# Performance work log

Hardware: AMD Instinct MI355X
Metric: run time of the kernel (lower is better)

The kernel has to match this reference:

```python
import jax, jax.numpy as jnp
import numpy as np

N, K, C_IN, C_OUT = 30000, 16, 128, 256


def setup_inputs() -> dict:
    key = jax.random.key(0)
    ks = jax.random.split(key, 8)
    s1 = 1.0 / np.sqrt(2 * C_IN)
    s2 = 1.0 / np.sqrt(C_OUT)
    s3 = 1.0 / np.sqrt(C_IN)
    return {
        "feat": jax.random.normal(ks[0], (N, C_IN), dtype=jnp.float32),
        "knn_idx": jax.random.randint(ks[1], (N, K), 0, N, dtype=jnp.int64),
        "W1": jax.random.uniform(ks[2], (2 * C_IN, C_OUT), jnp.float32, -s1, s1),
        "b1": jax.random.uniform(ks[3], (C_OUT,), jnp.float32, -s1, s1),
        "W2": jax.random.uniform(ks[4], (C_OUT, C_OUT), jnp.float32, -s2, s2),
        "b2": jax.random.uniform(ks[5], (C_OUT,), jnp.float32, -s2, s2),
        "Ws": jax.random.uniform(ks[6], (C_IN, C_OUT), jnp.float32, -s3, s3),
        "bs": jax.random.uniform(ks[7], (C_OUT,), jnp.float32, -s3, s3),
        "gamma": jnp.ones((C_OUT,), jnp.float32),
        "beta": jnp.zeros((C_OUT,), jnp.float32),
    }


def _layer_norm(x, gamma, beta, eps=1e-5):
    mu = jnp.mean(x, axis=-1, keepdims=True)
    var = jnp.var(x, axis=-1, keepdims=True)
    return (x - mu) * jax.lax.rsqrt(var + eps) * gamma + beta


def reference(feat, knn_idx, W1, b1, W2, b2, Ws, bs, gamma, beta):
    # gather neighbors: (N, K, C_in)
    neighbor = feat[knn_idx]
    center = feat[:, None, :]  # broadcast over K
    # edge feature: concat(center, neighbor - center) -> (N, K, 2*C_in)
    edge = jnp.concatenate([jnp.broadcast_to(center, neighbor.shape), neighbor - center], axis=-1)
    # edge MLP: Linear -> exact GELU -> Linear
    h = jax.nn.gelu(jnp.einsum("nkc,cd->nkd", edge, W1) + b1, approximate=False)
    edge_out = jnp.einsum("nkd,de->nke", h, W2) + b2  # (N, K, C_out)
    agg = jnp.max(edge_out, axis=1)  # (N, C_out)
    skip = feat @ Ws + bs
    return _layer_norm(agg + skip, gamma, beta)
```

## Files before the change

kernel.cpp:

```cpp
#include <hip/hip_runtime.h>
#include <hip/hip_bf16.h>
#include <math.h>

#define NPTS 30000
#define KNN  16
#define NB   30
#define GRID 250

typedef __attribute__((ext_vector_type(8)))  __bf16 bf16x8;
typedef __attribute__((ext_vector_type(16))) float  f32x16;
typedef __attribute__((ext_vector_type(4)))  float  f32x4;

__device__ __forceinline__ unsigned short f2bf(float x) {
    unsigned u = __builtin_bit_cast(unsigned, x);
    return (unsigned short)((u + 0x7FFFu + ((u >> 16) & 1u)) >> 16);
}
__device__ __forceinline__ float bf_lo(unsigned u) { return __builtin_bit_cast(float, u << 16); }
__device__ __forceinline__ float bf_hi(unsigned u) { return __builtin_bit_cast(float, u & 0xffff0000u); }
__device__ __forceinline__ unsigned pk2(float a, float b) {
    return (unsigned)f2bf(a) | ((unsigned)f2bf(b) << 16);
}
__device__ __forceinline__ float gelu_t(float x) {
    float x2 = x * x;
    float u  = x * fmaf(0.07135481624f, x2, 1.59576912161f);
    float e  = __expf(u);
    float r  = __builtin_amdgcn_rcpf(e + 1.0f);
    return fmaf(-x, r, x);
}

__global__ void prep_w(const float* __restrict__ W1, const float* __restrict__ W2,
                       const float* __restrict__ Ws,
                       unsigned short* __restrict__ w1dt, unsigned short* __restrict__ w2t,
                       unsigned short* __restrict__ wcst) {
    int t = blockIdx.x * 256 + threadIdx.x;
    {   int e = t >> 8, c = t & 255;
        w2t[t] = f2bf(W2[c * 256 + e]); }
    {   int col = t >> 7, k = t & 127;
        float v = (col < 256) ? W1[k * 256 + col] : Ws[k * 256 + (col - 256)];
        wcst[t] = f2bf(v); }
    if (t < 32768) {
        int d = t >> 7, k = t & 127;
        w1dt[t] = f2bf(W1[(128 + k) * 256 + d]); }
}

__global__ __launch_bounds__(512, 1) void edgeconv_main(
    const float* __restrict__ feat, const int* __restrict__ knn,
    const unsigned short* __restrict__ w1dt, const unsigned short* __restrict__ w2t,
    const unsigned short* __restrict__ wcst,
    const float* __restrict__ b1, const float* __restrict__ b2,
    const float* __restrict__ bs,
    const float* __restrict__ gamma, const float* __restrict__ beta,
    float* __restrict__ out)
{
    __shared__ __align__(16) unsigned char  s_edge[2][64 * 256];
    __shared__ __align__(16) unsigned char  s_h[64 * 512];
    __shared__ __align__(16) unsigned short s_c2[2][16][512];
    __shared__ __align__(16) float s_agg[2][4][256];

    const int lane = threadIdx.x & 63;
    const int wv   = threadIdx.x >> 6;
    const int l31  = lane & 31;
    const int lh   = lane >> 5;
    const int l15  = lane & 15;
    const int l4   = lane >> 4;
    const int pblock = blockIdx.x * 120;
    const int chb = wv * 32;

    bf16x8 w1f[8], w2f[16];
    #pragma unroll
    for (int ks = 0; ks < 8; ++ks)
        w1f[ks] = *(const bf16x8*)(w1dt + (chb + l31) * 128 + ks * 16 + lh * 8);
    #pragma unroll
    for (int ks = 0; ks < 16; ++ks)
        w2f[ks] = *(const bf16x8*)(w2t + (chb + l31) * 256 + ks * 16 + lh * 8);

    auto c2pass = [&](int s) {
        const int buf = s & 1;
        const int pb  = pblock + s * 16;
        bf16x8 af[4];
        #pragma unroll
        for (int ks = 0; ks < 4; ++ks) {
            int p = pb + l15; p = (p < NPTS) ? p : (NPTS - 1);
            const float* fp = feat + (long)p * 128 + ks * 32 + l4 * 8;
            float4 f0 = *(const float4*)fp;
            float4 f1 = *(const float4*)(fp + 4);
            uint4 u;
            u.x = pk2(f0.x, f0.y); u.y = pk2(f0.z, f0.w);
            u.z = pk2(f1.x, f1.y); u.w = pk2(f1.z, f1.w);
            af[ks] = __builtin_bit_cast(bf16x8, u);
        }
        #pragma unroll
        for (int j = 0; j < 8; ++j) {
            const int ct  = (wv - 4) * 8 + j;
            const int col = ct * 16 + l15;
            float bias = (ct < 16) ? b1[col] : (bs[col - 256] + b2[col - 256]);
            f32x4 acc = {bias, bias, bias, bias};
            #pragma unroll
            for (int ks = 0; ks < 4; ++ks) {
                bf16x8 bf = *(const bf16x8*)(wcst + col * 128 + ks * 32 + l4 * 8);
                acc = __builtin_amdgcn_mfma_f32_16x16x32_bf16(af[ks], bf, acc, 0, 0, 0);
            }
            #pragma unroll
            for (int r = 0; r < 4; ++r)
                s_c2[buf][l4 * 4 + r][col] = f2bf(acc[r]);
        }
    };

    auto stage = [&](int bt) {
        const int pt = wv >> 1;
        const int n  = pblock + bt * 4 + pt;
        const int kb = (wv & 1) * 8;
        float2 cc = *(const float2*)(feat + (long)n * 128 + lane * 2);
        int idx[8];
        #pragma unroll
        for (int kk = 0; kk < 8; ++kk) idx[kk] = knn[n * 16 + kb + kk];
        #pragma unroll
        for (int kk = 0; kk < 8; ++kk) {
            float2 nb = *(const float2*)(feat + (long)idx[kk] * 128 + lane * 2);
            int row = pt * 16 + kb + kk;
            unsigned v = pk2(nb.x - cc.x, nb.y - cc.y);
            *(unsigned*)(s_edge[bt & 1] + row * 256 + ((unsigned)(lane * 4) ^ (unsigned)((row & 7) << 4))) = v;
        }
    };

    stage(0);
    if (wv >= 4) c2pass(0);

    const f32x16 z16 = (f32x16)0.0f;

    #pragma unroll 1
    for (int i = 0; i <= NB; ++i) {
        if (i + 1 < NB) stage(i + 1);
        if ((i & 3) == 2 && ((i >> 2) + 1) < 8 && wv >= 4)
            c2pass((i >> 2) + 1);
        __syncthreads();

        if (i >= 1 && wv < 4) {
            const int bt2 = i - 1;
            const int n   = pblock + bt2 * 4 + wv;
            const int sB  = (bt2 >> 2) & 1;
            const int pt16 = (bt2 & 3) * 4 + wv;
            float4 ag = *(const float4*)&s_agg[bt2 & 1][wv][lane * 4];
            uint2 sk  = *(const uint2*)(&s_c2[sB][pt16][256 + lane * 4]);
            float x0 = ag.x + bf_lo(sk.x), x1 = ag.y + bf_hi(sk.x);
            float x2 = ag.z + bf_lo(sk.y), x3 = ag.w + bf_hi(sk.y);
            float s  = x0 + x1 + x2 + x3;
            float ss = fmaf(x0, x0, fmaf(x1, x1, fmaf(x2, x2, x3 * x3)));
            #pragma unroll
            for (int off = 1; off < 64; off <<= 1) {
                s  += __shfl_xor(s, off);
                ss += __shfl_xor(ss, off);
            }
            float mu   = s * (1.0f / 256.0f);
            float var  = ss * (1.0f / 256.0f) - mu * mu;
            float rstd = rsqrtf(var + 1e-5f);
            float4 g4 = *(const float4*)&gamma[lane * 4];
            float4 b4 = *(const float4*)&beta[lane * 4];
            float4 o;
            o.x = (x0 - mu) * rstd * g4.x + b4.x;
            o.y = (x1 - mu) * rstd * g4.y + b4.y;
            o.z = (x2 - mu) * rstd * g4.z + b4.z;
            o.w = (x3 - mu) * rstd * g4.w + b4.w;
            *(float4*)&out[(long)n * 256 + lane * 4] = o;
        }

        if (i < NB) {
            const int sB = (i >> 2) & 1;
            f32x16 acc1[2] = {z16, z16};
            #pragma unroll
            for (int rowb = 0; rowb < 2; ++rowb) {
                const int row = rowb * 32 + l31;
                const unsigned swz = (unsigned)((row & 7) << 4);
                const unsigned rb = (unsigned)row * 256u;
                #pragma unroll
                for (int ks = 0; ks < 8; ++ks) {
                    bf16x8 bf = *(const bf16x8*)(s_edge[i & 1] + rb + ((unsigned)(ks * 32 + lh * 16) ^ swz));
                    acc1[rowb] = __builtin_amdgcn_mfma_f32_32x32x16_bf16(w1f[ks], bf, acc1[rowb], 0, 0, 0);
                }
            }
            #pragma unroll
            for (int rowb = 0; rowb < 2; ++rowb) {
                const int row  = rowb * 32 + l31;
                const int pt16 = (i & 3) * 4 + rowb * 2 + (l31 >> 4);
                const unsigned swz = (unsigned)((row & 7) << 4);
                #pragma unroll
                for (int g = 0; g < 4; ++g) {
                    const int ch0 = chb + 8 * g + 4 * lh;
                    uint2 c2v = *(const uint2*)(&s_c2[sB][pt16][ch0]);
                    float v0 = gelu_t(acc1[rowb][4 * g + 0] + bf_lo(c2v.x));
                    float v1 = gelu_t(acc1[rowb][4 * g + 1] + bf_hi(c2v.x));
                    float v2 = gelu_t(acc1[rowb][4 * g + 2] + bf_lo(c2v.y));
                    float v3 = gelu_t(acc1[rowb][4 * g + 3] + bf_hi(c2v.y));
                    uint2 hv; hv.x = pk2(v0, v1); hv.y = pk2(v2, v3);
                    *(uint2*)(s_h + (unsigned)row * 512u + ((unsigned)(ch0 * 2) ^ swz)) = hv;
                }
            }
        }
        __syncthreads();

        if (i < NB) {
            #pragma unroll
            for (int rowb = 0; rowb < 2; ++rowb) {
                const int row = rowb * 32 + l31;
                const unsigned swz = (unsigned)((row & 7) << 4);
                const unsigned rb = (unsigned)row * 512u;
                f32x16 a2 = z16;
                #pragma unroll
                for (int ks = 0; ks < 16; ++ks) {
                    bf16x8 hf = *(const bf16x8*)(s_h + rb + ((unsigned)(ks * 32 + lh * 16) ^ swz));
                    a2 = __builtin_amdgcn_mfma_f32_32x32x16_bf16(hf, w2f[ks], a2, 0, 0, 0);
                }
                float m0 = a2[0], m1 = a2[8];
                #pragma unroll
                for (int r = 1; r < 8; ++r) {
                    m0 = fmaxf(m0, a2[r]);
                    m1 = fmaxf(m1, a2[8 + r]);
                }
                m0 = fmaxf(m0, __shfl_xor(m0, 32));
                m1 = fmaxf(m1, __shfl_xor(m1, 32));
                if (lh == 0) {
                    s_agg[i & 1][rowb * 2 + 0][chb + l31] = m0;
                    s_agg[i & 1][rowb * 2 + 1][chb + l31] = m1;
                }
            }
        }
    }
}

extern "C" void kernel_launch(void* const* d_in, const int* in_sizes, int n_in,
                              void* d_out, int out_size, void* d_ws, size_t ws_size,
                              hipStream_t stream) {
    const float* feat  = (const float*)d_in[0];
    const int*   knn   = (const int*)  d_in[1];
    const float* W1    = (const float*)d_in[2];
    const float* b1    = (const float*)d_in[3];
    const float* W2    = (const float*)d_in[4];
    const float* b2    = (const float*)d_in[5];
    const float* Ws    = (const float*)d_in[6];
    const float* bs    = (const float*)d_in[7];
    const float* gamma = (const float*)d_in[8];
    const float* beta  = (const float*)d_in[9];
    float* out = (float*)d_out;

    unsigned short* w1dt = (unsigned short*)d_ws;
    unsigned short* w2t  = w1dt + 32768;
    unsigned short* wcst = w2t + 65536;

    hipLaunchKernelGGL(prep_w, dim3(256), dim3(256), 0, stream, W1, W2, Ws, w1dt, w2t, wcst);
    hipLaunchKernelGGL(edgeconv_main, dim3(GRID), dim3(512), 0, stream,
                       feat, knn, w1dt, w2t, wcst, b1, b2, bs, gamma, beta, out);
}
```

Baseline: 205.8 us.

## Software-pipeline main loop with double-buffered hidden tile and one barrier per iteration

Restructures the main loop so that the second GEMM for the previous tile, the first GEMM and GELU for the current tile, and LayerNorm for the tile two back all run in one iteration. The hidden tile s_h is double-buffered, which drops one __syncthreads per iteration. Neighbor gathers are issued at the top of the iteration into registers and written to LDS at the end, so global latency overlaps the MFMA work. It also spreads the center/skip GEMM across all 8 waves, widens the LDS XOR swizzle, and uses the native bf16 conversion, at the cost of more LDS and register pressure.

New measurement: 201.9 us. About the same (-1.9%).

```diff
diff --git a/kernel.cpp b/kernel.cpp
--- a/kernel.cpp
+++ b/kernel.cpp
@@ -12,14 +12,14 @@
 typedef __attribute__((ext_vector_type(4)))  float  f32x4;
 
 __device__ __forceinline__ unsigned short f2bf(float x) {
-    unsigned u = __builtin_bit_cast(unsigned, x);
-    return (unsigned short)((u + 0x7FFFu + ((u >> 16) & 1u)) >> 16);
+    __bf16 b = (__bf16)x;
+    return __builtin_bit_cast(unsigned short, b);
+}
+__device__ __forceinline__ unsigned pk2(float a, float b) {
+    return (unsigned)f2bf(a) | ((unsigned)f2bf(b) << 16);
 }
 __device__ __forceinline__ float bf_lo(unsigned u) { return __builtin_bit_cast(float, u << 16); }
 __device__ __forceinline__ float bf_hi(unsigned u) { return __builtin_bit_cast(float, u & 0xffff0000u); }
-__device__ __forceinline__ unsigned pk2(float a, float b) {
-    return (unsigned)f2bf(a) | ((unsigned)f2bf(b) << 16);
-}
 __device__ __forceinline__ float gelu_t(float x) {
     float x2 = x * x;
     float u  = x * fmaf(0.07135481624f, x2, 1.59576912161f);
@@ -53,7 +53,7 @@
     float* __restrict__ out)
 {
     __shared__ __align__(16) unsigned char  s_edge[2][64 * 256];
-    __shared__ __align__(16) unsigned char  s_h[64 * 512];
+    __shared__ __align__(16) unsigned char  s_h[2][64 * 512];
     __shared__ __align__(16) unsigned short s_c2[2][16][512];
     __shared__ __align__(16) float s_agg[2][4][256];
 
@@ -90,8 +90,8 @@
             af[ks] = __builtin_bit_cast(bf16x8, u);
         }
         #pragma unroll
-        for (int j = 0; j < 8; ++j) {
-            const int ct  = (wv - 4) * 8 + j;
+        for (int j = 0; j < 4; ++j) {
+            const int ct  = wv * 4 + j;
             const int col = ct * 16 + l15;
             float bias = (ct < 16) ? b1[col] : (bs[col - 256] + b2[col - 256]);
             f32x4 acc = {bias, bias, bias, bias};
@@ -106,37 +106,104 @@
         }
     };
 
-    auto stage = [&](int bt) {
-        const int pt = wv >> 1;
-        const int n  = pblock + bt * 4 + pt;
-        const int kb = (wv & 1) * 8;
+    const int st_pt = wv >> 1;
+    const int st_kb = (wv & 1) * 8;
+
+    {
+        const int n = pblock + st_pt;
         float2 cc = *(const float2*)(feat + (long)n * 128 + lane * 2);
-        int idx[8];
-        #pragma unroll
-        for (int kk = 0; kk < 8; ++kk) idx[kk] = knn[n * 16 + kb + kk];
         #pragma unroll
         for (int kk = 0; kk < 8; ++kk) {
-            float2 nb = *(const float2*)(feat + (long)idx[kk] * 128 + lane * 2);
-            int row = pt * 16 + kb + kk;
+            int idx = knn[n * 16 + st_kb + kk];
+            float2 nb = *(const float2*)(feat + (long)idx * 128 + lane * 2);
+            int row = st_pt * 16 + st_kb + kk;
             unsigned v = pk2(nb.x - cc.x, nb.y - cc.y);
-            *(unsigned*)(s_edge[bt & 1] + row * 256 + ((unsigned)(lane * 4) ^ (unsigned)((row & 7) << 4))) = v;
-        }
-    };
-
-    stage(0);
-    if (wv >= 4) c2pass(0);
+            *(unsigned*)(s_edge[0] + row * 256 + ((unsigned)(lane * 4) ^ (unsigned)((row & 15) << 4))) = v;
+        }
+    }
+    c2pass(0);
+    __syncthreads();
 
     const f32x16 z16 = (f32x16)0.0f;
 
     #pragma unroll 1
-    for (int i = 0; i <= NB; ++i) {
-        if (i + 1 < NB) stage(i + 1);
-        if ((i & 3) == 2 && ((i >> 2) + 1) < 8 && wv >= 4)
-            c2pass((i >> 2) + 1);
-        __syncthreads();
-
-        if (i >= 1 && wv < 4) {
-            const int bt2 = i - 1;
+    for (int i = 0; i <= NB + 1; ++i) {
+        float2 cc; float2 nbr[8];
+        const bool doStage = (i + 1 < NB);
+        if (doStage) {
+            const int n = pblock + (i + 1) * 4 + st_pt;
+            cc = *(const float2*)(feat + (long)n * 128 + lane * 2);
+            int idx[8];
+            #pragma unroll
+            for (int kk = 0; kk < 8; ++kk) idx[kk] = knn[n * 16 + st_kb + kk];
+            #pragma unroll
+            for (int kk = 0; kk < 8; ++kk)
+                nbr[kk] = *(const float2*)(feat + (long)idx[kk] * 128 + lane * 2);
+        }
+
+        if (i >= 1 && i <= NB) {
+            const int bt = i - 1;
+            #pragma unroll
+            for (int rowb = 0; rowb < 2; ++rowb) {
+                const int row = rowb * 32 + l31;
+                const unsigned swz = (unsigned)((row & 31) << 4);
+                const unsigned rb = (unsigned)row * 512u;
+                f32x16 a2 = z16;
+                #pragma unroll
+                for (int ks = 0; ks < 16; ++ks) {
+                    bf16x8 hf = *(const bf16x8*)(s_h[bt & 1] + rb + ((unsigned)(ks * 32 + lh * 16) ^ swz));
+                    a2 = __builtin_amdgcn_mfma_f32_32x32x16_bf16(hf, w2f[ks], a2, 0, 0, 0);
+                }
+                float m0 = a2[0], m1 = a2[8];
+                #pragma unroll
+                for (int r = 1; r < 8; ++r) {
+                    m0 = fmaxf(m0, a2[r]);
+                    m1 = fmaxf(m1, a2[8 + r]);
+                }
+                m0 = fmaxf(m0, __shfl_xor(m0, 32));
+                m1 = fmaxf(m1, __shfl_xor(m1, 32));
+                if (lh == 0) {
+                    s_agg[bt & 1][rowb * 2 + 0][chb + l31] = m0;
+                    s_agg[bt & 1][rowb * 2 + 1][chb + l31] = m1;
+                }
+            }
+        }
+
+        if (i < NB) {
+            const int sB = (i >> 2) & 1;
+            f32x16 acc1[2] = {z16, z16};
+            #pragma unroll
+            for (int rowb = 0; rowb < 2; ++rowb) {
+                const int row = rowb * 32 + l31;
+                const unsigned swz = (unsigned)((row & 15) << 4);
+                const unsigned rb = (unsigned)row * 256u;
+                #pragma unroll
+                for (int ks = 0; ks < 8; ++ks) {
+                    bf16x8 bf = *(const bf16x8*)(s_edge[i & 1] + rb + ((unsigned)(ks * 32 + lh * 16) ^ swz));
+                    acc1[rowb] = __builtin_amdgcn_mfma_f32_32x32x16_bf16(w1f[ks], bf, acc1[rowb], 0, 0, 0);
+                }
+            }
+            #pragma unroll
+            for (int rowb = 0; rowb < 2; ++rowb) {
+                const int row  = rowb * 32 + l31;
+                const int pt16 = (i & 3) * 4 + rowb * 2 + (l31 >> 4);
+                const unsigned swz = (unsigned)((row & 31) << 4);
+                #pragma unroll
+                for (int g = 0; g < 4; ++g) {
+                    const int ch0 = chb + 8 * g + 4 * lh;
+                    uint2 c2v = *(const uint2*)(&s_c2[sB][pt16][ch0]);
+                    float v0 = gelu_t(acc1[rowb][4 * g + 0] + bf_lo(c2v.x));
+                    float v1 = gelu_t(acc1[rowb][4 * g + 1] + bf_hi(c2v.x));
+                    float v2 = gelu_t(acc1[rowb][4 * g + 2] + bf_lo(c2v.y));
+                    float v3 = gelu_t(acc1[rowb][4 * g + 3] + bf_hi(c2v.y));
+                    uint2 hv; hv.x = pk2(v0, v1); hv.y = pk2(v2, v3);
+                    *(uint2*)(s_h[i & 1] + (unsigned)row * 512u + ((unsigned)(ch0 * 2) ^ swz)) = hv;
+                }
+            }
+        }
+
+        if (i >= 2 && wv < 4) {
+            const int bt2 = i - 2;
             const int n   = pblock + bt2 * 4 + wv;
             const int sB  = (bt2 >> 2) & 1;
             const int pt16 = (bt2 & 3) * 4 + wv;
@@ -164,66 +231,21 @@
             *(float4*)&out[(long)n * 256 + lane * 4] = o;
         }
 
-        if (i < NB) {
-            const int sB = (i >> 2) & 1;
-            f32x16 acc1[2] = {z16, z16};
-            #pragma unroll
-            for (int rowb = 0; rowb < 2; ++rowb) {
-                const int row = rowb * 32 + l31;
-                const unsigned swz = (unsigned)((row & 7) << 4);
-                const unsigned rb = (unsigned)row * 256u;
-                #pragma unroll
-                for (int ks = 0; ks < 8; ++ks) {
-                    bf16x8 bf = *(const bf16x8*)(s_edge[i & 1] + rb + ((unsigned)(ks * 32 + lh * 16) ^ swz));
-                    acc1[rowb] = __builtin_amdgcn_mfma_f32_32x32x16_bf16(w1f[ks], bf, acc1[rowb], 0, 0, 0);
-                }
-            }
-            #pragma unroll
-            for (int rowb = 0; rowb < 2; ++rowb) {
-                const int row  = rowb * 32 + l31;
-                const int pt16 = (i & 3) * 4 + rowb * 2 + (l31 >> 4);
-                const unsigned swz = (unsigned)((row & 7) << 4);
-                #pragma unroll
-                for (int g = 0; g < 4; ++g) {
-                    const int ch0 = chb + 8 * g + 4 * lh;
-                    uint2 c2v = *(const uint2*)(&s_c2[sB][pt16][ch0]);
-                    float v0 = gelu_t(acc1[rowb][4 * g + 0] + bf_lo(c2v.x));
-                    float v1 = gelu_t(acc1[rowb][4 * g + 1] + bf_hi(c2v.x));
-                    float v2 = gelu_t(acc1[rowb][4 * g + 2] + bf_lo(c2v.y));
-                    float v3 = gelu_t(acc1[rowb][4 * g + 3] + bf_hi(c2v.y));
-                    uint2 hv; hv.x = pk2(v0, v1); hv.y = pk2(v2, v3);
-                    *(uint2*)(s_h + (unsigned)row * 512u + ((unsigned)(ch0 * 2) ^ swz)) = hv;
-                }
+        if ((i & 3) == 2) {
+            int s = (i + 2) >> 2;
+            if (s < 8) c2pass(s);
+        }
+
+        if (doStage) {
+            const int bt = i + 1;
+            #pragma unroll
+            for (int kk = 0; kk < 8; ++kk) {
+                int row = st_pt * 16 + st_kb + kk;
+                unsigned v = pk2(nbr[kk].x - cc.x, nbr[kk].y - cc.y);
+                *(unsigned*)(s_edge[bt & 1] + row * 256 + ((unsigned)(lane * 4) ^ (unsigned)((row & 15) << 4))) = v;
             }
         }
         __syncthreads();
-
-        if (i < NB) {
-            #pragma unroll
-            for (int rowb = 0; rowb < 2; ++rowb) {
-                const int row = rowb * 32 + l31;
-                const unsigned swz = (unsigned)((row & 7) << 4);
-                const unsigned rb = (unsigned)row * 512u;
-                f32x16 a2 = z16;
-                #pragma unroll
-                for (int ks = 0; ks < 16; ++ks) {
-                    bf16x8 hf = *(const bf16x8*)(s_h + rb + ((unsigned)(ks * 32 + lh * 16) ^ swz));
-                    a2 = __builtin_amdgcn_mfma_f32_32x32x16_bf16(hf, w2f[ks], a2, 0, 0, 0);
-                }
-                float m0 = a2[0], m1 = a2[8];
-                #pragma unroll
-                for (int r = 1; r < 8; ++r) {
-                    m0 = fmaxf(m0, a2[r]);
-                    m1 = fmaxf(m1, a2[8 + r]);
-                }
-                m0 = fmaxf(m0, __shfl_xor(m0, 32));
-                m1 = fmaxf(m1, __shfl_xor(m1, 32));
-                if (lh == 0) {
-                    s_agg[i & 1][rowb * 2 + 0][chb + l31] = m0;
-                    s_agg[i & 1][rowb * 2 + 1][chb + l31] = m1;
-                }
-            }
-        }
     }
 }
 
```
